# Kernel optimization log

Measured on AMD Instinct MI355X. Metric: run time of the kernel, lower is better.

## Reference

```python
import jax, jax.numpy as jnp
import numpy as np

H_DIM = 64
GRID = 8
NBR = 2.0
BN_EPS = 1e-5
N_SEQ = 64
N_PED = 64
BOTTLENECK = 1024


def setup_inputs() -> dict:
    key = jax.random.key(0)
    k0, k1, k2, k3 = jax.random.split(key, 4)
    batch = N_SEQ * N_PED
    h_states = jax.random.normal(k0, (1, batch, H_DIM), jnp.float32)
    # positions spread over a 4x4 area so some neighbors fall inside the 2.0 neighborhood
    end_pos = jax.random.uniform(k1, (batch, 2), jnp.float32) * 4.0
    rel_pos = jax.random.normal(k2, (batch, 2), jnp.float32)
    starts = jnp.arange(N_SEQ, dtype=jnp.int32) * N_PED
    seq_start_end = jnp.stack([starts, starts + N_PED], axis=1)
    in_dim = GRID * GRID * H_DIM  # 4096
    W = jax.random.normal(k3, (in_dim, BOTTLENECK), jnp.float32) / np.sqrt(in_dim)
    b = jnp.zeros((BOTTLENECK,), jnp.float32)
    gamma = jnp.ones((BOTTLENECK,), jnp.float32)
    beta = jnp.zeros((BOTTLENECK,), jnp.float32)
    return {"h_states": h_states, "seq_start_end": seq_start_end, "end_pos": end_pos,
            "rel_pos": rel_pos, "W": W, "b": b, "gamma": gamma, "beta": beta}


def _pool_scene(hidden, pos):
    # hidden: (n, h), pos: (n, 2). Pair (i, j): ped j binned into ped i's grid.
    n, h = hidden.shape
    g2 = GRID * GRID
    half = NBR / 2.0
    tl_x = pos[:, 0] - half
    tl_y = pos[:, 1] + half
    br_x = pos[:, 0] + half
    br_y = pos[:, 1] - half
    px = pos[None, :, 0]  # (1, n) -> broadcast over i
    py = pos[None, :, 1]
    cell_x = jnp.floor((px - tl_x[:, None]) / NBR * GRID)
    cell_y = jnp.floor((tl_y[:, None] - py) / NBR * GRID)
    grid = (cell_x + cell_y * GRID).astype(jnp.int32) + 1  # slot 0 = trash bin
    oob = ((px >= br_x[:, None]) | (px <= tl_x[:, None]) |
           (py >= tl_y[:, None]) | (py <= br_y[:, None]) |
           jnp.eye(n, dtype=bool))  # self-interaction excluded
    grid = grid + (jnp.arange(n, dtype=jnp.int32) * g2)[:, None]
    grid = jnp.where(oob, 0, grid)  # (n, n)
    src = jnp.broadcast_to(hidden[None], (n, n, h)).reshape(-1, h)
    buf = jnp.zeros((n * g2 + 1, h), hidden.dtype).at[grid.reshape(-1)].add(src)
    return buf[1:].reshape(n, g2 * h)


def reference(h_states, seq_start_end, end_pos, rel_pos, W, b, gamma, beta):
    batch = end_pos.shape[0]
    n_seq = seq_start_end.shape[0]
    n_ped = batch // n_seq  # equal-length scenes by construction
    hid = h_states.reshape(-1, H_DIM).reshape(n_seq, n_ped, H_DIM)
    pos = end_pos.reshape(n_seq, n_ped, 2)
    pool_h = jax.vmap(_pool_scene)(hid, pos).reshape(batch, -1)  # (batch, 4096)
    x = pool_h @ W + b
    # BatchNorm1d in training mode (batch statistics, biased variance)
    mean = jnp.mean(x, axis=0)
    var = jnp.var(x, axis=0)
    x = (x - mean) * jax.lax.rsqrt(var + BN_EPS) * gamma + beta
    return jax.nn.relu(x)
```

## Files before the change

kernel.cpp:

```cpp
#include <hip/hip_runtime.h>
#include <hip/hip_bf16.h>


#define NPED  64
#define BATCH 4096
#define HDIM  64
#define G2    64
#define KDIM  4096
#define NOUT  1024

typedef __attribute__((ext_vector_type(8))) short short8;
typedef __attribute__((ext_vector_type(4))) float f32x4;

__device__ __forceinline__ unsigned short f2bf(float f) {
    __hip_bfloat16 h = __float2bfloat16(f);
    return *reinterpret_cast<unsigned short*>(&h);
}

__device__ __forceinline__ void lds_load16(const void* g, void* l) {
    __builtin_amdgcn_global_load_lds(
        (const __attribute__((address_space(1))) void*)g,
        (__attribute__((address_space(3))) void*)l, 16, 0, 0);
}

__global__ __launch_bounds__(512) void pool_kernel(const float* __restrict__ h,
                                                   const float* __restrict__ pos,
                                                   unsigned short* __restrict__ A2) {
    __shared__ float hs[NPED * HDIM];
    __shared__ float pl[NPED * 2];
    int t = threadIdx.x;
    int w = t >> 6, lane = t & 63;
    int p0 = blockIdx.x * 8;
    int sbase = p0 & ~(NPED - 1);
    if (t < 128) pl[t] = pos[sbase * 2 + t];
    {
        const float4* src = (const float4*)(h + (size_t)sbase * HDIM);
        float4* dst = (float4*)hs;
        dst[t] = src[t];
        dst[t + 512] = src[t + 512];
    }
    __syncthreads();

    int i = p0 + w;
    int il = i & (NPED - 1);
    float cx0 = pl[2 * il], cy0 = pl[2 * il + 1];
    float tlx = cx0 - 1.f, tly = cy0 + 1.f, brx = cx0 + 1.f, bry = cy0 - 1.f;
    float px = pl[2 * lane], py = pl[2 * lane + 1];
    bool inb = (lane != il) && !(px >= brx || px <= tlx || py >= tly || py <= bry);
    int cellx = (int)floorf((px - tlx) * 4.f);
    int celly = (int)floorf((tly - py) * 4.f);
    int cell = cellx + celly * 8;
    inb = inb && ((unsigned)cell < 64u);

    int mtile = i >> 4, r = i & 15;
    unsigned short* outb = A2 + (size_t)mtile * 65536 + r * 8
                              + (lane >> 5) * 512 + ((lane >> 3) & 3) * 128 + (lane & 7);
    const float* hrow = hs + lane;
    #pragma unroll
    for (int c = 0; c < 64; ++c) {
        unsigned long long m = __ballot(inb && (cell == c));
        float a = 0.f;
        while (m) {
            int j = __builtin_ctzll(m);
            m &= m - 1;
            a += hrow[j * HDIM];
        }
        outb[c * 1024] = f2bf(a);
    }
}

__global__ __launch_bounds__(256) void wt_kernel(const float* __restrict__ W,
                                                 unsigned short* __restrict__ Wt,
                                                 float* __restrict__ stats) {
    __shared__ unsigned short tile[64][66];
    int k0 = blockIdx.x * 64;
    int n0 = blockIdx.y * 64;
    int t = threadIdx.x;
    if (blockIdx.x == 0 && blockIdx.y < 8) stats[blockIdx.y * 256 + t] = 0.f;
    #pragma unroll
    for (int p = 0; p < 4; ++p) {
        int lin = p * 256 + t;
        int c4 = lin & 15, kl = lin >> 4;
        float4 v = ((const float4*)(W + (size_t)(k0 + kl) * NOUT + n0))[c4];
        tile[c4 * 4 + 0][kl] = f2bf(v.x);
        tile[c4 * 4 + 1][kl] = f2bf(v.y);
        tile[c4 * 4 + 2][kl] = f2bf(v.z);
        tile[c4 * 4 + 3][kl] = f2bf(v.w);
    }
    __syncthreads();
    unsigned int* out = (unsigned int*)Wt;
    #pragma unroll
    for (int p = 0; p < 8; ++p) {
        int lin = p * 256 + t;
        int ku = lin & 31, nl = lin >> 5;
        unsigned int v = (unsigned int)tile[nl][2 * ku] |
                         ((unsigned int)tile[nl][2 * ku + 1] << 16);
        out[(size_t)(n0 + nl) * (KDIM / 2) + (k0 >> 1) + ku] = v;
    }
}

__global__ __launch_bounds__(256, 2) void gemm_kernel(const unsigned short* __restrict__ A2,
                                                      const unsigned short* __restrict__ Bt,
                                                      float* __restrict__ C,
                                                      float* __restrict__ P1,
                                                      float* __restrict__ P2,
                                                      float* __restrict__ P3) {
    __shared__ __align__(16) unsigned short Bs[128 * 64];
    int t = threadIdx.x;
    int w = t >> 6, lane = t & 63;
    int m0 = blockIdx.x * 256, n0 = blockIdx.y * 128;
    int kbase = blockIdx.z * 1024;
    int wm = w * 64;

    f32x4 acc[4][8];
    #pragma unroll
    for (int i = 0; i < 4; ++i)
        #pragma unroll
        for (int j = 0; j < 8; ++j)
            acc[i][j] = (f32x4){0.f, 0.f, 0.f, 0.f};

    int rbase = w * 32 + (lane >> 3);
    int koff = ((lane & 7) ^ (lane >> 3)) * 8;
    const unsigned short* Bg = Bt + (size_t)(n0 + rbase) * KDIM + kbase + koff;
    unsigned short* BsW = Bs + w * 2048 + lane * 8;

    const unsigned short* Abase = A2 + (size_t)((m0 + wm) >> 4) * 65536 + lane * 8;
    int ktile0 = kbase >> 5;

    for (int kt = 0; kt < 1024; kt += 64) {
        #pragma unroll
        for (int q = 0; q < 4; ++q)
            lds_load16(Bg + (size_t)q * 8 * KDIM + kt, BsW + q * 512);
        short8 af[2][4];
        int ktile = ktile0 + (kt >> 5);
        #pragma unroll
        for (int kk = 0; kk < 2; ++kk)
            #pragma unroll
            for (int i = 0; i < 4; ++i)
                af[kk][i] = *(const short8*)(Abase + ((size_t)i * 128 + ktile + kk) * 512);
        __syncthreads();
        #pragma unroll
        for (int kk = 0; kk < 2; ++kk) {
            int chunk = ((kk * 4 + (lane >> 4)) ^ (lane & 7)) * 8;
            #pragma unroll
            for (int j = 0; j < 8; ++j) {
                short8 b = *(const short8*)&Bs[(j * 16 + (lane & 15)) * 64 + chunk];
                #pragma unroll
                for (int i = 0; i < 4; ++i)
                    acc[i][j] = __builtin_amdgcn_mfma_f32_16x16x32_bf16(af[kk][i], b, acc[i][j], 0, 0, 0);
            }
        }
        __syncthreads();
    }

    float* dst = blockIdx.z == 0 ? C : blockIdx.z == 1 ? P1 : blockIdx.z == 2 ? P2 : P3;
    int col0 = n0 + (lane & 15);
    int row0 = m0 + wm + ((lane >> 4) << 2);
    #pragma unroll
    for (int i = 0; i < 4; ++i)
        #pragma unroll
        for (int j = 0; j < 8; ++j)
            #pragma unroll
            for (int r = 0; r < 4; ++r)
                dst[(size_t)(row0 + i * 16 + r) * NOUT + col0 + j * 16] = acc[i][j][r];
}

__global__ __launch_bounds__(256) void combine_stats(float* __restrict__ C,
                                                     const float* __restrict__ P1,
                                                     const float* __restrict__ P2,
                                                     const float* __restrict__ P3,
                                                     float* __restrict__ stats) {
    int t = threadIdx.x;
    int colchunk = blockIdx.x & 3;
    int rowchunk = blockIdx.x >> 2;
    int col = colchunk * 256 + t;
    size_t base = (size_t)rowchunk * 32 * NOUT + col;
    float s = 0.f, s2 = 0.f;
    #pragma unroll 4
    for (int r = 0; r < 32; ++r) {
        size_t ix = base + (size_t)r * NOUT;
        float v = (C[ix] + P1[ix]) + (P2[ix] + P3[ix]);
        C[ix] = v;
        s += v; s2 += v * v;
    }
    atomicAdd(&stats[col], s);
    atomicAdd(&stats[NOUT + col], s2);
}

__global__ __launch_bounds__(256) void norm_kernel(float* __restrict__ C,
                                                   const float* __restrict__ stats,
                                                   const float* __restrict__ gamma,
                                                   const float* __restrict__ beta) {
    int idx = blockIdx.x * 256 + threadIdx.x;
    int col4 = idx & 255;
    float4 x = ((const float4*)C)[idx];
    float4 s = ((const float4*)stats)[col4];
    float4 q = ((const float4*)(stats + NOUT))[col4];
    float4 g = ((const float4*)gamma)[col4];
    float4 b = ((const float4*)beta)[col4];
    const float inv_n = 1.f / 4096.f;
    float m, inv;
    m = s.x * inv_n; inv = rsqrtf(q.x * inv_n - m * m + 1e-5f); x.x = fmaxf((x.x - m) * inv * g.x + b.x, 0.f);
    m = s.y * inv_n; inv = rsqrtf(q.y * inv_n - m * m + 1e-5f); x.y = fmaxf((x.y - m) * inv * g.y + b.y, 0.f);
    m = s.z * inv_n; inv = rsqrtf(q.z * inv_n - m * m + 1e-5f); x.z = fmaxf((x.z - m) * inv * g.z + b.z, 0.f);
    m = s.w * inv_n; inv = rsqrtf(q.w * inv_n - m * m + 1e-5f); x.w = fmaxf((x.w - m) * inv * g.w + b.w, 0.f);
    ((float4*)C)[idx] = x;
}

extern "C" void kernel_launch(void* const* d_in, const int* in_sizes, int n_in,
                              void* d_out, int out_size, void* d_ws, size_t ws_size,
                              hipStream_t stream) {
    const float* h      = (const float*)d_in[0];
    const float* endpos = (const float*)d_in[2];
    const float* W      = (const float*)d_in[4];
    const float* gamma  = (const float*)d_in[6];
    const float* beta   = (const float*)d_in[7];
    float* C = (float*)d_out;

    char* ws = (char*)d_ws;
    size_t off = 0;
    unsigned short* A2 = (unsigned short*)(ws + off); off += (size_t)BATCH * KDIM * 2;
    unsigned short* Wt = (unsigned short*)(ws + off); off += (size_t)NOUT * KDIM * 2;
    float* P1 = (float*)(ws + off); off += (size_t)BATCH * NOUT * 4;
    float* P2 = (float*)(ws + off); off += (size_t)BATCH * NOUT * 4;
    float* P3 = (float*)(ws + off); off += (size_t)BATCH * NOUT * 4;
    float* stats = (float*)(ws + off);

    pool_kernel<<<BATCH / 8, 512, 0, stream>>>(h, endpos, A2);
    wt_kernel<<<dim3(KDIM / 64, NOUT / 64), 256, 0, stream>>>(W, Wt, stats);
    gemm_kernel<<<dim3(BATCH / 256, NOUT / 128, 4), 256, 0, stream>>>(A2, Wt, C, P1, P2, P3);
    combine_stats<<<512, 256, 0, stream>>>(C, P1, P2, P3, stats);
    norm_kernel<<<(BATCH * NOUT / 4) / 256, 256, 0, stream>>>(C, stats, gamma, beta);
}
```

Before: 150.9 us.

## Fuse pool and weight-transpose kernels, double-buffer GEMM B tiles, store split-K partials as bf16

The pooling and weight-conversion kernels are merged into one launch, with block index choosing the role, so a launch is saved and the two can overlap. The GEMM moves to 128x128 block tiles with a 2x2 wave layout and double-buffered LDS loads of B, allowing three blocks per SM and overlapping the next tile's load with the current MFMAs. Split-K partials 1-3 are written as bf16 instead of fp32, halving their write and read traffic in the combine step at some cost in accuracy.

```diff
diff --git a/kernel.cpp b/kernel.cpp
--- a/kernel.cpp
+++ b/kernel.cpp
@@ -16,6 +16,10 @@
     __hip_bfloat16 h = __float2bfloat16(f);
     return *reinterpret_cast<unsigned short*>(&h);
 }
+__device__ __forceinline__ float bf2f(unsigned short u) {
+    unsigned int v = ((unsigned int)u) << 16;
+    return __builtin_bit_cast(float, v);
+}
 
 __device__ __forceinline__ void lds_load16(const void* g, void* l) {
     __builtin_amdgcn_global_load_lds(
@@ -23,152 +27,173 @@
         (__attribute__((address_space(3))) void*)l, 16, 0, 0);
 }
 
-__global__ __launch_bounds__(512) void pool_kernel(const float* __restrict__ h,
+__global__ __launch_bounds__(512) void prep_kernel(const float* __restrict__ h,
                                                    const float* __restrict__ pos,
-                                                   unsigned short* __restrict__ A2) {
-    __shared__ float hs[NPED * HDIM];
-    __shared__ float pl[NPED * 2];
+                                                   unsigned short* __restrict__ A2,
+                                                   const float* __restrict__ W,
+                                                   unsigned short* __restrict__ Wt,
+                                                   float* __restrict__ stats) {
+    __shared__ __align__(16) char smem[2 * 64 * 66 * 2 + 1024];
+    int t = threadIdx.x;
+    if (blockIdx.x < 512) {
+        float* hs = (float*)smem;
+        float* pl = (float*)(smem + NPED * HDIM * 4);
+        int w = t >> 6, lane = t & 63;
+        int p0 = blockIdx.x * 8;
+        int sbase = p0 & ~(NPED - 1);
+        if (t < 128) pl[t] = pos[sbase * 2 + t];
+        {
+            const float4* src = (const float4*)(h + (size_t)sbase * HDIM);
+            float4* dst = (float4*)hs;
+            dst[t] = src[t];
+            dst[t + 512] = src[t + 512];
+        }
+        __syncthreads();
+
+        int i = p0 + w;
+        int il = i & (NPED - 1);
+        float cx0 = pl[2 * il], cy0 = pl[2 * il + 1];
+        float tlx = cx0 - 1.f, tly = cy0 + 1.f, brx = cx0 + 1.f, bry = cy0 - 1.f;
+        float px = pl[2 * lane], py = pl[2 * lane + 1];
+        bool inb = (lane != il) && !(px >= brx || px <= tlx || py >= tly || py <= bry);
+        int cellx = (int)floorf((px - tlx) * 4.f);
+        int celly = (int)floorf((tly - py) * 4.f);
+        int cell = cellx + celly * 8;
+        inb = inb && ((unsigned)cell < 64u);
+
+        int mtile = i >> 4, r = i & 15;
+        unsigned short* outb = A2 + (size_t)mtile * 65536 + r * 8
+                                  + (lane >> 5) * 512 + ((lane >> 3) & 3) * 128 + (lane & 7);
+        const float* hrow = hs + lane;
+        #pragma unroll
+        for (int c = 0; c < 64; ++c) {
+            unsigned long long m = __ballot(inb && (cell == c));
+            float a = 0.f;
+            while (m) {
+                int j = __builtin_ctzll(m);
+                m &= m - 1;
+                a += hrow[j * HDIM];
+            }
+            outb[c * 1024] = f2bf(a);
+        }
+    } else {
+        int wid = blockIdx.x - 512;
+        int half = t >> 8, tt = t & 255;
+        int o = wid * 2 + half;
+        int bx = o & 63, by = o >> 6;
+        unsigned short (*tile)[66] = (unsigned short (*)[66])(smem + half * 64 * 66 * 2);
+        int k0 = bx * 64, n0 = by * 64;
+        if (bx == 0 && by < 8) stats[by * 256 + tt] = 0.f;
+        #pragma unroll
+        for (int p = 0; p < 4; ++p) {
+            int lin = p * 256 + tt;
+            int c4 = lin & 15, kl = lin >> 4;
+            float4 v = ((const float4*)(W + (size_t)(k0 + kl) * NOUT + n0))[c4];
+            tile[c4 * 4 + 0][kl] = f2bf(v.x);
+            tile[c4 * 4 + 1][kl] = f2bf(v.y);
+            tile[c4 * 4 + 2][kl] = f2bf(v.z);
+            tile[c4 * 4 + 3][kl] = f2bf(v.w);
+        }
+        __syncthreads();
+        unsigned int* out = (unsigned int*)Wt;
+        #pragma unroll
+        for (int p = 0; p < 8; ++p) {
+            int lin = p * 256 + tt;
+            int ku = lin & 31, nl = lin >> 5;
+            unsigned int v = (unsigned int)tile[nl][2 * ku] |
+                             ((unsigned int)tile[nl][2 * ku + 1] << 16);
+            out[(size_t)(n0 + nl) * (KDIM / 2) + (k0 >> 1) + ku] = v;
+        }
+    }
+}
+
+__global__ __launch_bounds__(256, 3) void gemm_kernel(const unsigned short* __restrict__ A2,
+                                                      const unsigned short* __restrict__ Bt,
+                                                      float* __restrict__ C,
+                                                      unsigned short* __restrict__ P1,
+                                                      unsigned short* __restrict__ P2,
+                                                      unsigned short* __restrict__ P3) {
+    __shared__ __align__(16) unsigned short Bs[2][128 * 64];
     int t = threadIdx.x;
     int w = t >> 6, lane = t & 63;
-    int p0 = blockIdx.x * 8;
-    int sbase = p0 & ~(NPED - 1);
-    if (t < 128) pl[t] = pos[sbase * 2 + t];
-    {
-        const float4* src = (const float4*)(h + (size_t)sbase * HDIM);
-        float4* dst = (float4*)hs;
-        dst[t] = src[t];
-        dst[t + 512] = src[t + 512];
-    }
-    __syncthreads();
-
-    int i = p0 + w;
-    int il = i & (NPED - 1);
-    float cx0 = pl[2 * il], cy0 = pl[2 * il + 1];
-    float tlx = cx0 - 1.f, tly = cy0 + 1.f, brx = cx0 + 1.f, bry = cy0 - 1.f;
-    float px = pl[2 * lane], py = pl[2 * lane + 1];
-    bool inb = (lane != il) && !(px >= brx || px <= tlx || py >= tly || py <= bry);
-    int cellx = (int)floorf((px - tlx) * 4.f);
-    int celly = (int)floorf((tly - py) * 4.f);
-    int cell = cellx + celly * 8;
-    inb = inb && ((unsigned)cell < 64u);
-
-    int mtile = i >> 4, r = i & 15;
-    unsigned short* outb = A2 + (size_t)mtile * 65536 + r * 8
-                              + (lane >> 5) * 512 + ((lane >> 3) & 3) * 128 + (lane & 7);
-    const float* hrow = hs + lane;
-    #pragma unroll
-    for (int c = 0; c < 64; ++c) {
-        unsigned long long m = __ballot(inb && (cell == c));
-        float a = 0.f;
-        while (m) {
-            int j = __builtin_ctzll(m);
-            m &= m - 1;
-            a += hrow[j * HDIM];
-        }
-        outb[c * 1024] = f2bf(a);
-    }
-}
-
-__global__ __launch_bounds__(256) void wt_kernel(const float* __restrict__ W,
-                                                 unsigned short* __restrict__ Wt,
-                                                 float* __restrict__ stats) {
-    __shared__ unsigned short tile[64][66];
-    int k0 = blockIdx.x * 64;
-    int n0 = blockIdx.y * 64;
-    int t = threadIdx.x;
-    if (blockIdx.x == 0 && blockIdx.y < 8) stats[blockIdx.y * 256 + t] = 0.f;
-    #pragma unroll
-    for (int p = 0; p < 4; ++p) {
-        int lin = p * 256 + t;
-        int c4 = lin & 15, kl = lin >> 4;
-        float4 v = ((const float4*)(W + (size_t)(k0 + kl) * NOUT + n0))[c4];
-        tile[c4 * 4 + 0][kl] = f2bf(v.x);
-        tile[c4 * 4 + 1][kl] = f2bf(v.y);
-        tile[c4 * 4 + 2][kl] = f2bf(v.z);
-        tile[c4 * 4 + 3][kl] = f2bf(v.w);
-    }
-    __syncthreads();
-    unsigned int* out = (unsigned int*)Wt;
-    #pragma unroll
-    for (int p = 0; p < 8; ++p) {
-        int lin = p * 256 + t;
-        int ku = lin & 31, nl = lin >> 5;
-        unsigned int v = (unsigned int)tile[nl][2 * ku] |
-                         ((unsigned int)tile[nl][2 * ku + 1] << 16);
-        out[(size_t)(n0 + nl) * (KDIM / 2) + (k0 >> 1) + ku] = v;
-    }
-}
-
-__global__ __launch_bounds__(256, 2) void gemm_kernel(const unsigned short* __restrict__ A2,
-                                                      const unsigned short* __restrict__ Bt,
-                                                      float* __restrict__ C,
-                                                      float* __restrict__ P1,
-                                                      float* __restrict__ P2,
-                                                      float* __restrict__ P3) {
-    __shared__ __align__(16) unsigned short Bs[128 * 64];
-    int t = threadIdx.x;
-    int w = t >> 6, lane = t & 63;
-    int m0 = blockIdx.x * 256, n0 = blockIdx.y * 128;
+    int m0 = blockIdx.x * 128, n0 = blockIdx.y * 128;
     int kbase = blockIdx.z * 1024;
-    int wm = w * 64;
-
-    f32x4 acc[4][8];
+    int wm = (w >> 1) * 64, wn = (w & 1) * 64;
+
+    f32x4 acc[4][4];
     #pragma unroll
     for (int i = 0; i < 4; ++i)
         #pragma unroll
-        for (int j = 0; j < 8; ++j)
+        for (int j = 0; j < 4; ++j)
             acc[i][j] = (f32x4){0.f, 0.f, 0.f, 0.f};
 
     int rbase = w * 32 + (lane >> 3);
     int koff = ((lane & 7) ^ (lane >> 3)) * 8;
     const unsigned short* Bg = Bt + (size_t)(n0 + rbase) * KDIM + kbase + koff;
-    unsigned short* BsW = Bs + w * 2048 + lane * 8;
+    int ldsoff = w * 2048 + lane * 8;
 
     const unsigned short* Abase = A2 + (size_t)((m0 + wm) >> 4) * 65536 + lane * 8;
-    int ktile0 = kbase >> 5;
-
-    for (int kt = 0; kt < 1024; kt += 64) {
-        #pragma unroll
-        for (int q = 0; q < 4; ++q)
-            lds_load16(Bg + (size_t)q * 8 * KDIM + kt, BsW + q * 512);
+    int K50 = kbase >> 5;
+
+    #pragma unroll
+    for (int q = 0; q < 4; ++q)
+        lds_load16(Bg + (size_t)q * 8 * KDIM, &Bs[0][0] + ldsoff + q * 512);
+
+    for (int kt = 0; kt < 16; ++kt) {
+        __syncthreads();
+        if (kt + 1 < 16) {
+            #pragma unroll
+            for (int q = 0; q < 4; ++q)
+                lds_load16(Bg + (size_t)q * 8 * KDIM + (kt + 1) * 64,
+                           &Bs[(kt + 1) & 1][0] + ldsoff + q * 512);
+        }
         short8 af[2][4];
-        int ktile = ktile0 + (kt >> 5);
+        int K5 = K50 + kt * 2;
         #pragma unroll
         for (int kk = 0; kk < 2; ++kk)
             #pragma unroll
             for (int i = 0; i < 4; ++i)
-                af[kk][i] = *(const short8*)(Abase + ((size_t)i * 128 + ktile + kk) * 512);
-        __syncthreads();
+                af[kk][i] = *(const short8*)(Abase + ((size_t)i * 128 + K5 + kk) * 512);
+        const unsigned short* Bc = &Bs[kt & 1][0];
         #pragma unroll
         for (int kk = 0; kk < 2; ++kk) {
             int chunk = ((kk * 4 + (lane >> 4)) ^ (lane & 7)) * 8;
             #pragma unroll
-            for (int j = 0; j < 8; ++j) {
-                short8 b = *(const short8*)&Bs[(j * 16 + (lane & 15)) * 64 + chunk];
+            for (int j = 0; j < 4; ++j) {
+                short8 b = *(const short8*)&Bc[(wn + j * 16 + (lane & 15)) * 64 + chunk];
                 #pragma unroll
                 for (int i = 0; i < 4; ++i)
                     acc[i][j] = __builtin_amdgcn_mfma_f32_16x16x32_bf16(af[kk][i], b, acc[i][j], 0, 0, 0);
             }
         }
-        __syncthreads();
-    }
-
-    float* dst = blockIdx.z == 0 ? C : blockIdx.z == 1 ? P1 : blockIdx.z == 2 ? P2 : P3;
-    int col0 = n0 + (lane & 15);
+    }
+
+    int col0 = n0 + wn + (lane & 15);
     int row0 = m0 + wm + ((lane >> 4) << 2);
-    #pragma unroll
-    for (int i = 0; i < 4; ++i)
-        #pragma unroll
-        for (int j = 0; j < 8; ++j)
-            #pragma unroll
-            for (int r = 0; r < 4; ++r)
-                dst[(size_t)(row0 + i * 16 + r) * NOUT + col0 + j * 16] = acc[i][j][r];
+    if (blockIdx.z == 0) {
+        #pragma unroll
+        for (int i = 0; i < 4; ++i)
+            #pragma unroll
+            for (int j = 0; j < 4; ++j)
+                #pragma unroll
+                for (int r = 0; r < 4; ++r)
+                    C[(size_t)(row0 + i * 16 + r) * NOUT + col0 + j * 16] = acc[i][j][r];
+    } else {
+        unsigned short* dst = blockIdx.z == 1 ? P1 : blockIdx.z == 2 ? P2 : P3;
+        #pragma unroll
+        for (int i = 0; i < 4; ++i)
+            #pragma unroll
+            for (int j = 0; j < 4; ++j)
+                #pragma unroll
+                for (int r = 0; r < 4; ++r)
+                    dst[(size_t)(row0 + i * 16 + r) * NOUT + col0 + j * 16] = f2bf(acc[i][j][r]);
+    }
 }
 
 __global__ __launch_bounds__(256) void combine_stats(float* __restrict__ C,
-                                                     const float* __restrict__ P1,
-                                                     const float* __restrict__ P2,
-                                                     const float* __restrict__ P3,
+                                                     const unsigned short* __restrict__ P1,
+                                                     const unsigned short* __restrict__ P2,
+                                                     const unsigned short* __restrict__ P3,
                                                      float* __restrict__ stats) {
     int t = threadIdx.x;
     int colchunk = blockIdx.x & 3;
@@ -179,7 +204,7 @@
     #pragma unroll 4
     for (int r = 0; r < 32; ++r) {
         size_t ix = base + (size_t)r * NOUT;
-        float v = (C[ix] + P1[ix]) + (P2[ix] + P3[ix]);
+        float v = C[ix] + bf2f(P1[ix]) + bf2f(P2[ix]) + bf2f(P3[ix]);
         C[ix] = v;
         s += v; s2 += v * v;
     }
@@ -221,14 +246,13 @@
     size_t off = 0;
     unsigned short* A2 = (unsigned short*)(ws + off); off += (size_t)BATCH * KDIM * 2;
     unsigned short* Wt = (unsigned short*)(ws + off); off += (size_t)NOUT * KDIM * 2;
-    float* P1 = (float*)(ws + off); off += (size_t)BATCH * NOUT * 4;
-    float* P2 = (float*)(ws + off); off += (size_t)BATCH * NOUT * 4;
-    float* P3 = (float*)(ws + off); off += (size_t)BATCH * NOUT * 4;
+    unsigned short* P1 = (unsigned short*)(ws + off); off += (size_t)BATCH * NOUT * 2;
+    unsigned short* P2 = (unsigned short*)(ws + off); off += (size_t)BATCH * NOUT * 2;
+    unsigned short* P3 = (unsigned short*)(ws + off); off += (size_t)BATCH * NOUT * 2;
     float* stats = (float*)(ws + off);
 
-    pool_kernel<<<BATCH / 8, 512, 0, stream>>>(h, endpos, A2);
-    wt_kernel<<<dim3(KDIM / 64, NOUT / 64), 256, 0, stream>>>(W, Wt, stats);
-    gemm_kernel<<<dim3(BATCH / 256, NOUT / 128, 4), 256, 0, stream>>>(A2, Wt, C, P1, P2, P3);
+    prep_kernel<<<1024, 512, 0, stream>>>(h, endpos, A2, W, Wt, stats);
+    gemm_kernel<<<dim3(BATCH / 128, NOUT / 128, 4), 256, 0, stream>>>(A2, Wt, C, P1, P2, P3);
     combine_stats<<<512, 256, 0, stream>>>(C, P1, P2, P3, stats);
     norm_kernel<<<(BATCH * NOUT / 4) / 256, 256, 0, stream>>>(C, stats, gamma, beta);
 }
```

Result: no change. 153.5 us (+1.7%).
